# Performance work log

Hardware: AMD Instinct MI355X
Metric: run time of the kernel (lower is better)

## Reference

```python
import jax, jax.numpy as jnp
import numpy as np

EMBED = 1024
D_FF = 4 * EMBED
N_EXPERTS = 8
TOP_K = 2
B, S = 2, 1024


def setup_inputs() -> dict:
    key = jax.random.key(0)
    ks = jax.random.split(key, 10)
    sc_d = 1.0 / np.sqrt(EMBED)
    sc_h = 1.0 / np.sqrt(D_FF)
    return {
        "inputs": jax.random.normal(ks[0], (B, S, EMBED), jnp.float32),
        # router MLP: Linear(D,4D) -> ReLU -> Linear(4D,E)
        "rw1": jax.random.normal(ks[1], (EMBED, D_FF), jnp.float32) * sc_d,
        "rb1": jnp.zeros((D_FF,), jnp.float32),
        "rw2": jax.random.normal(ks[2], (D_FF, N_EXPERTS), jnp.float32) * sc_h,
        "rb2": jnp.zeros((N_EXPERTS,), jnp.float32),
        # stacked expert weights: Linear(D,4D) -> ReLU -> Linear(4D,D)
        "W1": jax.random.normal(ks[3], (N_EXPERTS, EMBED, D_FF), jnp.float32) * sc_d,
        "b1": jnp.zeros((N_EXPERTS, D_FF), jnp.float32),
        "W2": jax.random.normal(ks[4], (N_EXPERTS, D_FF, EMBED), jnp.float32) * sc_h,
        "b2": jnp.zeros((N_EXPERTS, EMBED), jnp.float32),
    }


def reference(inputs, rw1, rb1, rw2, rb2, W1, b1, W2, b2):
    Bb, Ss, D = inputs.shape
    T = Bb * Ss
    xf = inputs.reshape(T, D)  # [T, D]

    # Router: scores over experts, keep top-k, softmax over kept entries only.
    score = jax.nn.relu(xf @ rw1 + rb1) @ rw2 + rb2          # [T, E]
    _, topi = jax.lax.top_k(score, TOP_K)                    # [T, K]
    mask = jnp.zeros(score.shape, bool).at[jnp.arange(T)[:, None], topi].set(True)
    gate = jax.nn.softmax(jnp.where(mask, score, -jnp.inf), axis=-1)  # [T, E]

    # Dense per-expert MLP weighted by gate; gate==0 for non-top-k experts,
    # matching the original masked gather/scatter exactly.
    out = jnp.zeros_like(xf)
    for e in range(N_EXPERTS):
        h = jax.nn.relu(xf @ W1[e] + b1[e])                  # [T, 4D]
        y = h @ W2[e] + b2[e]                                # [T, D]
        out = out + gate[:, e:e + 1] * y
    return out.reshape(Bb, Ss, D)
```

## Files before the change

### kernel.cpp

```cpp
#include <hip/hip_runtime.h>
#include <stdint.h>

typedef unsigned short ushort_t;
typedef __attribute__((ext_vector_type(8))) short short8;
typedef __attribute__((ext_vector_type(4))) float f32x4;

#define EMBED   1024
#define DFF     4096
#define NEXP    8
#define TOKENS  2048
#define SLOTS   4096
#define TMAX    40
#define TG      ((TMAX + 7) / 8)

__device__ __forceinline__ ushort_t f2bf(float f) {
  unsigned u = __float_as_uint(f);
  u += 0x7FFFu + ((u >> 16) & 1u);
  return (ushort_t)(u >> 16);
}
__device__ __forceinline__ float bf2f(ushort_t b) {
  return __uint_as_float(((unsigned)b) << 16);
}

__device__ __forceinline__ void gl2lds16(const void* g, void* l) {
  typedef const __attribute__((address_space(1))) unsigned char* gp_t;
  typedef __attribute__((address_space(3))) unsigned char* lp_t;
  __builtin_amdgcn_global_load_lds((gp_t)(uintptr_t)g, (lp_t)(uintptr_t)l, 16, 0, 0);
}

__device__ __forceinline__ void transp_body(const float* __restrict__ src,
                                            ushort_t* __restrict__ dst,
                                            int src_ld, int dst_ld, int bx, int by,
                                            int dst_koff, int lo, float (*t)[65])
{
  int n0 = bx * 64, k0 = by * 64;
  int tid = threadIdx.x;
  int kk = tid >> 4, nn = (tid & 15) * 4;
  #pragma unroll
  for (int it = 0; it < 4; it++) {
    float4 v = *(const float4*)(src + (size_t)(k0 + kk + it * 16) * src_ld + n0 + nn);
    t[kk + it * 16][nn]     = v.x;
    t[kk + it * 16][nn + 1] = v.y;
    t[kk + it * 16][nn + 2] = v.z;
    t[kk + it * 16][nn + 3] = v.w;
  }
  __syncthreads();
  int nn2 = tid >> 3, kk2 = (tid & 7) * 8;
  #pragma unroll
  for (int it = 0; it < 2; it++) {
    int n = nn2 + it * 32;
    union { ushort_t u[8]; uint4 v; } pk;
    #pragma unroll
    for (int j = 0; j < 8; j++) {
      float xv = t[kk2 + j][n];
      ushort_t hv = f2bf(xv);
      pk.u[j] = lo ? f2bf(xv - bf2f(hv)) : hv;
    }
    *(uint4*)(dst + (size_t)(n0 + n) * dst_ld + dst_koff + k0 + kk2) = pk.v;
  }
}

__global__ void transp_conv(const float* __restrict__ src, ushort_t* __restrict__ dst,
                            int src_ld, int dst_ld, long src_estride, long dst_estride,
                            int dst_koff, int lo)
{
  __shared__ __align__(16) float t[64][65];
  transp_body(src + (size_t)blockIdx.z * src_estride,
              dst + (size_t)blockIdx.z * dst_estride,
              src_ld, dst_ld, blockIdx.x, blockIdx.y, dst_koff, lo, t);
}

__global__ __launch_bounds__(256) void prep_kernel(const float* __restrict__ x,
    ushort_t* __restrict__ Xs, const float* __restrict__ rw1,
    ushort_t* __restrict__ RW1t, int* __restrict__ counts)
{
  __shared__ __align__(16) float tt[64][65];
  int bid = blockIdx.x;
  if (bid < TOKENS) {
    if (bid == 0 && threadIdx.x < NEXP) counts[threadIdx.x] = 0;
    int d = threadIdx.x * 4;
    float4 v = *(const float4*)(x + (size_t)bid * EMBED + d);
    ushort4 hi, lo;
    hi.x = f2bf(v.x); lo.x = f2bf(v.x - bf2f(hi.x));
    hi.y = f2bf(v.y); lo.y = f2bf(v.y - bf2f(hi.y));
    hi.z = f2bf(v.z); lo.z = f2bf(v.z - bf2f(hi.z));
    hi.w = f2bf(v.w); lo.w = f2bf(v.w - bf2f(hi.w));
    ushort_t* row = Xs + (size_t)bid * 2048;
    *(ushort4*)(row + d)        = hi;
    *(ushort4*)(row + 1024 + d) = lo;
    return;
  }
  int idx = bid - TOKENS;
  int n0 = (idx & 63) * 64, k0 = (idx >> 6) * 64;
  int tid = threadIdx.x;
  int kk = tid >> 4, nn = (tid & 15) * 4;
  #pragma unroll
  for (int it = 0; it < 4; it++) {
    float4 v = *(const float4*)(rw1 + (size_t)(k0 + kk + it * 16) * DFF + n0 + nn);
    tt[kk + it * 16][nn]     = v.x;
    tt[kk + it * 16][nn + 1] = v.y;
    tt[kk + it * 16][nn + 2] = v.z;
    tt[kk + it * 16][nn + 3] = v.w;
  }
  __syncthreads();
  int nn2 = tid >> 3, kk2 = (tid & 7) * 8;
  #pragma unroll
  for (int it = 0; it < 2; it++) {
    int n = nn2 + it * 32;
    union { ushort_t u[8]; uint4 v; } ph, pl;
    #pragma unroll
    for (int j = 0; j < 8; j++) {
      float xv = tt[kk2 + j][n];
      ushort_t hv = f2bf(xv);
      ph.u[j] = hv;
      pl.u[j] = f2bf(xv - bf2f(hv));
    }
    ushort_t* row = RW1t + (size_t)(n0 + n) * 3072 + k0 + kk2;
    *(uint4*)(row)        = ph.v;
    *(uint4*)(row + 1024) = ph.v;
    *(uint4*)(row + 2048) = pl.v;
  }
}

template<int APATH, int OUTMODE, bool RELU, bool EXPERT, int SPLITK, int NX, int TSHAPE>
__global__ __launch_bounds__(256, 3)
void gemm_kernel(const ushort_t* __restrict__ A, const ushort_t* __restrict__ B,
                 const float* __restrict__ bias, void* __restrict__ Cout,
                 const float* __restrict__ slot_gate, const int* __restrict__ slot_token,
                 const int* __restrict__ off, const int* __restrict__ tile_e,
                 const int* __restrict__ tile_y, int e0, int e1,
                 int M, int N, int K, int ngb,
                 const float* __restrict__ tsrc, ushort_t* __restrict__ tdst)
{
  __shared__ __align__(16) char lds_raw[49152];
  auto As = (ushort_t(*)[4096])lds_raw;
  auto Bs = (ushort_t(*)[4096])(lds_raw + 24576);

  if constexpr (TSHAPE > 0) {
    int bidf = blockIdx.x;
    if (bidf >= ngb) {
      int idx = bidf - ngb;
      auto tt = (float(*)[65])lds_raw;
      const size_t ES = (size_t)EMBED * DFF;
      if constexpr (TSHAPE == 1) {
        int bx = idx & 63, by = (idx >> 6) & 15, z = idx >> 10;
        transp_body(tsrc + z * ES, tdst + z * ES, DFF, EMBED, bx, by, 0, 0, tt);
      } else {
        int bx = idx & 15, by = (idx >> 4) & 63, z = idx >> 10;
        transp_body(tsrc + z * ES, tdst + z * ES, EMBED, DFF, bx, by, 0, 0, tt);
      }
      return;
    }
  }

  int e = 0, kc = 0, row0, col0, m_base, m_cnt;
  if (EXPERT) {
    constexpr int INNER = NX * SPLITK;
    int bid = blockIdx.x;
    int xcd = bid & 7;
    int j   = bid >> 3;
    int t   = xcd + 8 * (j / INNER);
    int i   = j % INNER;
    int xi  = i % NX;
    kc      = i / NX;
    e = tile_e[t];
    if (e < e0 || e >= e1) return;
    row0   = tile_y[t] * 128;
    col0   = xi * 128;
    m_base = off[e];
    m_cnt  = off[e + 1] - m_base;
  } else {
    int bid = blockIdx.x;
    row0 = (bid >> 5) * 128;
    col0 = (bid & 31) * 128;
    m_base = 0; m_cnt = M;
    if (row0 >= m_cnt) return;
  }
  const int Kc   = K / SPLITK;
  const int kbeg = kc * Kc;

  const int tid  = threadIdx.x;
  const int lane = tid & 63;
  const int wid  = tid >> 6;
  const int wm = wid & 1, wn = wid >> 1;

  const int srow  = lane >> 2;
  const int schk8 = ((lane & 3) ^ ((lane >> 3) & 3)) * 8;

  const ushort_t* gA[2];
  const ushort_t* gB[2];
  int aoff[2];
  const ushort_t* Bt = B + (EXPERT ? (size_t)(e - e0) * (size_t)N * K : 0);
  #pragma unroll
  for (int h = 0; h < 2; h++) {
    int r  = row0 + h * 64 + wid * 16 + srow;
    int rl = min(r, m_cnt - 1);
    size_t rowb;
    if (APATH == 2)      rowb = (size_t)slot_token[m_base + rl] * 2048;
    else if (APATH == 1) rowb = (size_t)rl * 2048;
    else                 rowb = (size_t)(m_base + rl) * (size_t)K;
    gA[h]   = A + rowb + (APATH == 0 ? kbeg : 0) + schk8;
    aoff[h] = (h * 64 + wid * 16) * 32;

    int n = col0 + h * 64 + wid * 16 + srow;
    gB[h] = Bt + (size_t)n * K + kbeg + schk8;
  }

  auto stage = [&](int pb, int kt) {
    const int k0 = kt << 5;
    const int k0a = (APATH == 1 && k0 >= 2048) ? k0 - 2048 : k0;
    #pragma unroll
    for (int h = 0; h < 2; h++) {
      gl2lds16(gA[h] + k0a, &As[pb][aoff[h]]);
      gl2lds16(gB[h] + k0,  &Bs[pb][aoff[h]]);
    }
  };

  f32x4 acc[4][4];
  #pragma unroll
  for (int i = 0; i < 4; i++)
    #pragma unroll
    for (int j = 0; j < 4; j++)
      acc[i][j] = (f32x4){0.f, 0.f, 0.f, 0.f};

  const int q  = lane >> 4;
  const int rr = lane & 15;
  const int sw8 = (q ^ ((rr >> 1) & 3)) * 8;
  const int abase = (wm * 64 + rr) * 32 + sw8;
  const int bbase = (wn * 64 + rr) * 32 + sw8;

  const int nkt = Kc >> 5;

  stage(0, 0);
  if (nkt > 1) stage(1, 1);

  for (int kt = 0; kt < nkt; kt++) {
    if (kt + 1 < nkt) asm volatile("s_waitcnt vmcnt(4)" ::: "memory");
    else              asm volatile("s_waitcnt vmcnt(0)" ::: "memory");
    __builtin_amdgcn_s_barrier();
    __builtin_amdgcn_sched_barrier(0);
    if (kt + 2 < nkt) stage((kt + 2) % 3, kt + 2);

    const int cur = kt % 3;
    short8 af[4], bfr[4];
    #pragma unroll
    for (int i = 0; i < 4; i++) {
      af[i]  = *(const short8*)(&As[cur][abase + i * 512]);
      bfr[i] = *(const short8*)(&Bs[cur][bbase + i * 512]);
    }
    asm volatile("s_waitcnt lgkmcnt(0)" ::: "memory");
    __builtin_amdgcn_sched_barrier(0);
    #pragma unroll
    for (int mt = 0; mt < 4; mt++)
      #pragma unroll
      for (int nt = 0; nt < 4; nt++)
        acc[mt][nt] = __builtin_amdgcn_mfma_f32_16x16x32_bf16(af[mt], bfr[nt], acc[mt][nt], 0, 0, 0);
  }

  const float* biasp = bias + (EXPERT ? (size_t)e * N : 0);
  float bv[4];
  #pragma unroll
  for (int nt = 0; nt < 4; nt++)
    bv[nt] = biasp[col0 + wn * 64 + nt * 16 + rr];
  const float bscale = (SPLITK == 1 || kc == 0) ? 1.f : 0.f;

  if constexpr (OUTMODE == 4) {
    const float* rw2p = slot_gate;
    float4 wa[4], wb[4];
    #pragma unroll
    for (int nt = 0; nt < 4; nt++) {
      int c = col0 + wn * 64 + nt * 16 + rr;
      wa[nt] = *(const float4*)(rw2p + (size_t)c * 8);
      wb[nt] = *(const float4*)(rw2p + (size_t)c * 8 + 4);
    }
    float* Ps = (float*)Cout;
    const int xi2 = (col0 >> 6) + wn;
    #pragma unroll
    for (int mt = 0; mt < 4; mt++) {
      #pragma unroll
      for (int i = 0; i < 4; i++) {
        float4 sA = {0.f, 0.f, 0.f, 0.f}, sB = {0.f, 0.f, 0.f, 0.f};
        #pragma unroll
        for (int nt = 0; nt < 4; nt++) {
          float v = acc[mt][nt][i] + bv[nt];
          if (RELU) v = fmaxf(v, 0.f);
          sA.x += v * wa[nt].x; sA.y += v * wa[nt].y;
          sA.z += v * wa[nt].z; sA.w += v * wa[nt].w;
          sB.x += v * wb[nt].x; sB.y += v * wb[nt].y;
          sB.z += v * wb[nt].z; sB.w += v * wb[nt].w;
        }
        #pragma unroll
        for (int o = 1; o <= 8; o <<= 1) {
          sA.x += __shfl_xor(sA.x, o); sA.y += __shfl_xor(sA.y, o);
          sA.z += __shfl_xor(sA.z, o); sA.w += __shfl_xor(sA.w, o);
          sB.x += __shfl_xor(sB.x, o); sB.y += __shfl_xor(sB.y, o);
          sB.z += __shfl_xor(sB.z, o); sB.w += __shfl_xor(sB.w, o);
        }
        if (rr == 0) {
          int row = row0 + wm * 64 + mt * 16 + q * 4 + i;
          float* p = Ps + ((size_t)row * 64 + xi2) * 8;
          *(float4*)p       = sA;
          *(float4*)(p + 4) = sB;
        }
      }
    }
  } else {
    #pragma unroll
    for (int mt = 0; mt < 4; mt++) {
      #pragma unroll
      for (int i = 0; i < 4; i++) {
        int r_loc = row0 + wm * 64 + mt * 16 + q * 4 + i;
        if (r_loc < m_cnt) {
          int slot = m_base + r_loc;
          float g = 1.f;
          if (OUTMODE == 3) g = slot_gate[slot];
          #pragma unroll
          for (int nt = 0; nt < 4; nt++) {
            float v = acc[mt][nt][i] + bscale * bv[nt];
            if (RELU) v = fmaxf(v, 0.f);
            int c = col0 + wn * 64 + nt * 16 + rr;
            if (OUTMODE == 0)      ((float*)Cout)[(size_t)slot * N + c]    = v;
            else if (OUTMODE == 1) ((ushort_t*)Cout)[(size_t)slot * N + c] = f2bf(v);
            else ((float*)Cout)[((size_t)kc * SLOTS + slot) * N + c] = g * v;
          }
        }
      }
    }
  }
}

__global__ void router_reduce(const float* __restrict__ Ps, const float* __restrict__ rb2,
                              int* __restrict__ topi, float* __restrict__ gates,
                              int* __restrict__ counts)
{
  int t = blockIdx.x * 4 + (threadIdx.x >> 6);
  if (t >= TOKENS) return;
  int lane = threadIdx.x & 63;
  const float* pt = Ps + (size_t)t * 512;
  float4 v0 = *(const float4*)(pt + lane * 8);
  float4 v1 = *(const float4*)(pt + lane * 8 + 4);
  #pragma unroll
  for (int o = 1; o <= 32; o <<= 1) {
    v0.x += __shfl_xor(v0.x, o); v0.y += __shfl_xor(v0.y, o);
    v0.z += __shfl_xor(v0.z, o); v0.w += __shfl_xor(v0.w, o);
    v1.x += __shfl_xor(v1.x, o); v1.y += __shfl_xor(v1.y, o);
    v1.z += __shfl_xor(v1.z, o); v1.w += __shfl_xor(v1.w, o);
  }
  if (lane == 0) {
    float s[8] = {v0.x + rb2[0], v0.y + rb2[1], v0.z + rb2[2], v0.w + rb2[3],
                  v1.x + rb2[4], v1.y + rb2[5], v1.z + rb2[6], v1.w + rb2[7]};
    int i0 = 0;
    #pragma unroll
    for (int e = 1; e < 8; e++) if (s[e] > s[i0]) i0 = e;
    int i1 = (i0 == 0) ? 1 : 0;
    #pragma unroll
    for (int e = 0; e < 8; e++) if (e != i0 && s[e] > s[i1]) i1 = e;
    float ex = __expf(s[i1] - s[i0]);
    float g0 = 1.f / (1.f + ex);
    float g1 = ex / (1.f + ex);
    topi[t * 2] = i0; topi[t * 2 + 1] = i1;
    gates[t * 2] = g0; gates[t * 2 + 1] = g1;
    atomicAdd(&counts[i0], 1);
    atomicAdd(&counts[i1], 1);
  }
}

__global__ void assign_all(const int* __restrict__ counts, const int* __restrict__ topi,
                           const float* __restrict__ gates, int* __restrict__ off,
                           int* __restrict__ tile_e, int* __restrict__ tile_y,
                           int* __restrict__ slot_token, float* __restrict__ slot_gate,
                           int* __restrict__ tok_slot)
{
  __shared__ int s_off[NEXP];
  __shared__ int s_cur[NEXP];
  int tid = threadIdx.x;
  if (tid < NEXP) s_cur[tid] = 0;
  if (tid == 0) {
    int a = 0, t = 0;
    for (int e = 0; e < NEXP; e++) {
      off[e] = a; s_off[e] = a;
      int c = counts[e]; a += c;
      int ty = (c + 127) >> 7;
      for (int y = 0; y < ty; y++) { tile_e[t] = e; tile_y[t] = y; t++; }
    }
    off[NEXP] = a;
    for (; t < TMAX; t++) { tile_e[t] = -1; tile_y[t] = 0; }
  }
  __syncthreads();
  for (int t = tid; t < TOKENS; t += 256) {
    #pragma unroll
    for (int k = 0; k < 2; k++) {
      int e = topi[t * 2 + k];
      int p = atomicAdd(&s_cur[e], 1);
      int s = s_off[e] + p;
      slot_token[s] = t;
      slot_gate[s]  = gates[t * 2 + k];
      tok_slot[t * 2 + k] = s;
    }
  }
}

template<int NC>
__global__ void combine_out(const float* __restrict__ Ys, const int* __restrict__ tok_slot,
                            float* __restrict__ out)
{
  int t = blockIdx.x;
  int d = threadIdx.x * 4;
  int s0 = tok_slot[t * 2], s1 = tok_slot[t * 2 + 1];
  float4 o = {0.f, 0.f, 0.f, 0.f};
  #pragma unroll
  for (int k = 0; k < NC; k++) {
    float4 a = *(const float4*)(Ys + ((size_t)k * SLOTS + s0) * EMBED + d);
    float4 b = *(const float4*)(Ys + ((size_t)k * SLOTS + s1) * EMBED + d);
    o.x += a.x + b.x;
    o.y += a.y + b.y;
    o.z += a.z + b.z;
    o.w += a.w + b.w;
  }
  *(float4*)(out + (size_t)t * EMBED + d) = o;
}

extern "C" void kernel_launch(void* const* d_in, const int* in_sizes, int n_in,
                              void* d_out, int out_size, void* d_ws, size_t ws_size,
                              hipStream_t stream)
{
  const float* x   = (const float*)d_in[0];
  const float* rw1 = (const float*)d_in[1];
  const float* rb1 = (const float*)d_in[2];
  const float* rw2 = (const float*)d_in[3];
  const float* rb2 = (const float*)d_in[4];
  const float* W1  = (const float*)d_in[5];
  const float* b1  = (const float*)d_in[6];
  const float* W2  = (const float*)d_in[7];
  const float* b2  = (const float*)d_in[8];
  float* out = (float*)d_out;
  char* ws = (char*)d_ws;

  const long W1ES = (long)EMBED * DFF;
  const long W2ES = (long)DFF * EMBED;
  const size_t SZ_R = (size_t)4096 * 4096 * 2;

  const bool FULL = ws_size >= ((size_t)300 << 20);

  if (FULL) {
    char* p = ws;
    ushort_t* W1T  = (ushort_t*)p;  p += (size_t)NEXP * DFF * EMBED * 2;
    ushort_t* W2T  = (ushort_t*)p;  p += (size_t)NEXP * EMBED * DFF * 2;
    ushort_t* RW1t = (ushort_t*)p;  p += (size_t)4096 * 3072 * 2;
    ushort_t* Hs   = (ushort_t*)p;  p += (size_t)SLOTS * DFF * 2;
    ushort_t* Xhl  = (ushort_t*)p;  p += (size_t)TOKENS * 2048 * 2;
    float*    Ys   = (float*)p;     p += (size_t)2 * SLOTS * EMBED * 4;
    float*    Ps   = (float*)p;     p += (size_t)TOKENS * 512 * 4;
    int*   topi       = (int*)p;    p += TOKENS * 2 * 4;
    float* gates      = (float*)p;  p += TOKENS * 2 * 4;
    int*   tok_slot   = (int*)p;    p += TOKENS * 2 * 4;
    int*   slot_token = (int*)p;    p += SLOTS * 4;
    float* slot_gate  = (float*)p;  p += SLOTS * 4;
    int*   counts     = (int*)p;    p += 256;
    int*   off        = (int*)p;    p += 256;
    int*   tile_e     = (int*)p;    p += 256;
    int*   tile_y     = (int*)p;    p += 256;

    prep_kernel<<<TOKENS + 1024, 256, 0, stream>>>(x, Xhl, rw1, RW1t, counts);

    gemm_kernel<1, 4, true, false, 1, 32, 1>
        <<<dim3(512 + 8192, 1, 1), 256, 0, stream>>>(Xhl, RW1t, rb1, Ps, rw2,
            nullptr, nullptr, nullptr, nullptr, 0, NEXP, TOKENS, DFF, 3072,
            512, W1, W1T);

    router_reduce<<<512, 256, 0, stream>>>(Ps, rb2, topi, gates, counts);
    assign_all<<<1, 256, 0, stream>>>(counts, topi, gates, off, tile_e, tile_y,
                                      slot_token, slot_gate, tok_slot);

    gemm_kernel<2, 1, true, true, 1, 32, 2>
        <<<dim3(8 * TG * 32 + 8192, 1, 1), 256, 0, stream>>>(Xhl, W1T, b1, Hs,
            nullptr, slot_token, off, tile_e, tile_y, 0, NEXP, 0, DFF, EMBED,
            8 * TG * 32, W2, W2T);

    gemm_kernel<0, 3, false, true, 2, 8, 0>
        <<<dim3(8 * TG * 16, 1, 1), 256, 0, stream>>>(Hs, W2T, b2, Ys,
            slot_gate, nullptr, off, tile_e, tile_y, 0, NEXP, 0, EMBED, DFF,
            0, nullptr, nullptr);

    combine_out<2><<<TOKENS, 256, 0, stream>>>(Ys, tok_slot, out);
  } else {
    ushort_t* RW1t = (ushort_t*)ws;
    ushort_t* WT   = (ushort_t*)ws;
    ushort_t* Hs   = (ushort_t*)(ws + SZ_R);
    ushort_t* Xhl  = (ushort_t*)(ws + 2 * SZ_R);
    float*    Ys   = (float*)(ws + 2 * SZ_R);
    char* p = ws + 3 * SZ_R;
    float* Ps         = (float*)p;  p += (size_t)TOKENS * 512 * 4;
    int*   topi       = (int*)p;    p += TOKENS * 2 * 4;
    float* gates      = (float*)p;  p += TOKENS * 2 * 4;
    int*   tok_slot   = (int*)p;    p += TOKENS * 2 * 4;
    int*   slot_token = (int*)p;    p += SLOTS * 4;
    float* slot_gate  = (float*)p;  p += SLOTS * 4;
    int*   counts     = (int*)p;    p += 256;
    int*   off        = (int*)p;    p += 256;
    int*   tile_e     = (int*)p;    p += 256;
    int*   tile_y     = (int*)p;    p += 256;

    prep_kernel<<<TOKENS + 1024, 256, 0, stream>>>(x, Xhl, rw1, RW1t, counts);

    gemm_kernel<1, 4, true, false, 1, 32, 0>
        <<<dim3(512, 1, 1), 256, 0, stream>>>(Xhl, RW1t, rb1, Ps, rw2, nullptr,
            nullptr, nullptr, nullptr, 0, NEXP, TOKENS, DFF, 3072,
            0, nullptr, nullptr);
    router_reduce<<<512, 256, 0, stream>>>(Ps, rb2, topi, gates, counts);
    assign_all<<<1, 256, 0, stream>>>(counts, topi, gates, off, tile_e, tile_y,
                                      slot_token, slot_gate, tok_slot);

    for (int half = 0; half < 2; half++) {
      int e0 = half * 4;
      transp_conv<<<dim3(64, 16, 4), 256, 0, stream>>>(W1 + (size_t)e0 * W1ES, WT,
          DFF, EMBED, W1ES, W1ES, 0, 0);
      gemm_kernel<2, 1, true, true, 1, 32, 0>
          <<<dim3(8 * TG * 32, 1, 1), 256, 0, stream>>>(Xhl, WT, b1, Hs,
              nullptr, slot_token, off, tile_e, tile_y, e0, e0 + 4, 0, DFF, EMBED,
              0, nullptr, nullptr);
    }
    for (int half = 0; half < 2; half++) {
      int e0 = half * 4;
      transp_conv<<<dim3(16, 64, 4), 256, 0, stream>>>(W2 + (size_t)e0 * W2ES, WT,
          EMBED, DFF, W2ES, W2ES, 0, 0);
      gemm_kernel<0, 3, false, true, 2, 8, 0>
          <<<dim3(8 * TG * 16, 1, 1), 256, 0, stream>>>(Hs, WT, b2, Ys,
              slot_gate, nullptr, off, tile_e, tile_y, e0, e0 + 4, 0, EMBED, DFF,
              0, nullptr, nullptr);
    }

    combine_out<2><<<TOKENS, 256, 0, stream>>>(Ys, tok_slot, out);
  }
}
```

Before: 553.9 us.

## Fuse router top-k and slot assignment into router GEMM via last-block atomics

Removes the separate router_reduce and assign_all launches. The last of each 32-block group of the router GEMM, detected with an atomic counter, reduces partial scores and does top-2 and gating for its 128 tokens. The last of those 16 group-finisher blocks then builds the expert offsets, tile lists and slot maps. This saves two kernel launches and their serialization gaps, at the cost of a serial tail on a few blocks. It also relies on threadfence ordering and counters reset in prep_kernel.

New measurement: 657.3 us. 1.19x slower.

```diff
diff --git a/kernel.cpp b/kernel.cpp
--- a/kernel.cpp
+++ b/kernel.cpp
@@ -77,7 +77,7 @@
   __shared__ __align__(16) float tt[64][65];
   int bid = blockIdx.x;
   if (bid < TOKENS) {
-    if (bid == 0 && threadIdx.x < NEXP) counts[threadIdx.x] = 0;
+    if (bid == 0 && threadIdx.x < 64) counts[threadIdx.x] = 0;
     int d = threadIdx.x * 4;
     float4 v = *(const float4*)(x + (size_t)bid * EMBED + d);
     ushort4 hi, lo;
@@ -130,9 +130,13 @@
                  const int* __restrict__ off, const int* __restrict__ tile_e,
                  const int* __restrict__ tile_y, int e0, int e1,
                  int M, int N, int K, int ngb,
-                 const float* __restrict__ tsrc, ushort_t* __restrict__ tdst)
+                 const float* __restrict__ tsrc, ushort_t* __restrict__ tdst,
+                 const float* __restrict__ r_rb2, int* r_topi, float* r_gates,
+                 int* r_tok_slot, int* r_slot_token, float* r_slot_gate,
+                 int* r_counts, int* r_off, int* r_tile_e, int* r_tile_y)
 {
   __shared__ __align__(16) char lds_raw[49152];
+  __shared__ int s_role;
   auto As = (ushort_t(*)[4096])lds_raw;
   auto Bs = (ushort_t(*)[4096])(lds_raw + 24576);
 
@@ -304,6 +308,78 @@
         }
       }
     }
+
+    __threadfence();
+    __syncthreads();
+    const int rg = (int)(blockIdx.x >> 5);
+    if (tid == 0)
+      s_role = (atomicAdd(&r_counts[16 + rg], 1) == 31);
+    __syncthreads();
+    if (s_role) {
+      __threadfence();
+      for (int it = 0; it < 32; it++) {
+        int t = rg * 128 + it * 4 + (tid >> 6);
+        const float* pt = Ps + (size_t)t * 512;
+        float4 v0 = *(const float4*)(pt + lane * 8);
+        float4 v1 = *(const float4*)(pt + lane * 8 + 4);
+        #pragma unroll
+        for (int o = 1; o <= 32; o <<= 1) {
+          v0.x += __shfl_xor(v0.x, o); v0.y += __shfl_xor(v0.y, o);
+          v0.z += __shfl_xor(v0.z, o); v0.w += __shfl_xor(v0.w, o);
+          v1.x += __shfl_xor(v1.x, o); v1.y += __shfl_xor(v1.y, o);
+          v1.z += __shfl_xor(v1.z, o); v1.w += __shfl_xor(v1.w, o);
+        }
+        if (lane == 0) {
+          float s[8] = {v0.x + r_rb2[0], v0.y + r_rb2[1], v0.z + r_rb2[2], v0.w + r_rb2[3],
+                        v1.x + r_rb2[4], v1.y + r_rb2[5], v1.z + r_rb2[6], v1.w + r_rb2[7]};
+          int i0 = 0;
+          #pragma unroll
+          for (int ee = 1; ee < 8; ee++) if (s[ee] > s[i0]) i0 = ee;
+          int i1 = (i0 == 0) ? 1 : 0;
+          #pragma unroll
+          for (int ee = 0; ee < 8; ee++) if (ee != i0 && s[ee] > s[i1]) i1 = ee;
+          float ex = __expf(s[i1] - s[i0]);
+          r_topi[t * 2] = i0; r_topi[t * 2 + 1] = i1;
+          r_gates[t * 2] = 1.f / (1.f + ex); r_gates[t * 2 + 1] = ex / (1.f + ex);
+          atomicAdd(&r_counts[i0], 1);
+          atomicAdd(&r_counts[i1], 1);
+        }
+      }
+      __threadfence();
+      __syncthreads();
+      if (tid == 0)
+        s_role = (atomicAdd(&r_counts[32], 1) == 15);
+      __syncthreads();
+      if (s_role) {
+        __threadfence();
+        int* s_off = (int*)lds_raw;
+        int* s_cur = (int*)lds_raw + 8;
+        if (tid < NEXP) s_cur[tid] = 0;
+        if (tid == 0) {
+          int a = 0, t = 0;
+          for (int ee = 0; ee < NEXP; ee++) {
+            r_off[ee] = a; s_off[ee] = a;
+            int c = r_counts[ee]; a += c;
+            int ty = (c + 127) >> 7;
+            for (int y = 0; y < ty; y++) { r_tile_e[t] = ee; r_tile_y[t] = y; t++; }
+          }
+          r_off[NEXP] = a;
+          for (; t < TMAX; t++) { r_tile_e[t] = -1; r_tile_y[t] = 0; }
+        }
+        __syncthreads();
+        for (int t = tid; t < TOKENS; t += 256) {
+          #pragma unroll
+          for (int k = 0; k < 2; k++) {
+            int ee = r_topi[t * 2 + k];
+            int pp = atomicAdd(&s_cur[ee], 1);
+            int s = s_off[ee] + pp;
+            r_slot_token[s] = t;
+            r_slot_gate[s]  = r_gates[t * 2 + k];
+            r_tok_slot[t * 2 + k] = s;
+          }
+        }
+      }
+    }
   } else {
     #pragma unroll
     for (int mt = 0; mt < 4; mt++) {
@@ -325,77 +401,6 @@
           }
         }
       }
-    }
-  }
-}
-
-__global__ void router_reduce(const float* __restrict__ Ps, const float* __restrict__ rb2,
-                              int* __restrict__ topi, float* __restrict__ gates,
-                              int* __restrict__ counts)
-{
-  int t = blockIdx.x * 4 + (threadIdx.x >> 6);
-  if (t >= TOKENS) return;
-  int lane = threadIdx.x & 63;
-  const float* pt = Ps + (size_t)t * 512;
-  float4 v0 = *(const float4*)(pt + lane * 8);
-  float4 v1 = *(const float4*)(pt + lane * 8 + 4);
-  #pragma unroll
-  for (int o = 1; o <= 32; o <<= 1) {
-    v0.x += __shfl_xor(v0.x, o); v0.y += __shfl_xor(v0.y, o);
-    v0.z += __shfl_xor(v0.z, o); v0.w += __shfl_xor(v0.w, o);
-    v1.x += __shfl_xor(v1.x, o); v1.y += __shfl_xor(v1.y, o);
-    v1.z += __shfl_xor(v1.z, o); v1.w += __shfl_xor(v1.w, o);
-  }
-  if (lane == 0) {
-    float s[8] = {v0.x + rb2[0], v0.y + rb2[1], v0.z + rb2[2], v0.w + rb2[3],
-                  v1.x + rb2[4], v1.y + rb2[5], v1.z + rb2[6], v1.w + rb2[7]};
-    int i0 = 0;
-    #pragma unroll
-    for (int e = 1; e < 8; e++) if (s[e] > s[i0]) i0 = e;
-    int i1 = (i0 == 0) ? 1 : 0;
-    #pragma unroll
-    for (int e = 0; e < 8; e++) if (e != i0 && s[e] > s[i1]) i1 = e;
-    float ex = __expf(s[i1] - s[i0]);
-    float g0 = 1.f / (1.f + ex);
-    float g1 = ex / (1.f + ex);
-    topi[t * 2] = i0; topi[t * 2 + 1] = i1;
-    gates[t * 2] = g0; gates[t * 2 + 1] = g1;
-    atomicAdd(&counts[i0], 1);
-    atomicAdd(&counts[i1], 1);
-  }
-}
-
-__global__ void assign_all(const int* __restrict__ counts, const int* __restrict__ topi,
-                           const float* __restrict__ gates, int* __restrict__ off,
-                           int* __restrict__ tile_e, int* __restrict__ tile_y,
-                           int* __restrict__ slot_token, float* __restrict__ slot_gate,
-                           int* __restrict__ tok_slot)
-{
-  __shared__ int s_off[NEXP];
-  __shared__ int s_cur[NEXP];
-  int tid = threadIdx.x;
-  if (tid < NEXP) s_cur[tid] = 0;
-  if (tid == 0) {
-    int a = 0, t = 0;
-    for (int e = 0; e < NEXP; e++) {
-      off[e] = a; s_off[e] = a;
-      int c = counts[e]; a += c;
-      int ty = (c + 127) >> 7;
-      for (int y = 0; y < ty; y++) { tile_e[t] = e; tile_y[t] = y; t++; }
-    }
-    off[NEXP] = a;
-    for (; t < TMAX; t++) { tile_e[t] = -1; tile_y[t] = 0; }
-  }
-  __syncthreads();
-  for (int t = tid; t < TOKENS; t += 256) {
-    #pragma unroll
-    for (int k = 0; k < 2; k++) {
-      int e = topi[t * 2 + k];
-      int p = atomicAdd(&s_cur[e], 1);
-      int s = s_off[e] + p;
-      slot_token[s] = t;
-      slot_gate[s]  = gates[t * 2 + k];
-      tok_slot[t * 2 + k] = s;
     }
   }
 }
@@ -466,21 +471,23 @@
     gemm_kernel<1, 4, true, false, 1, 32, 1>
         <<<dim3(512 + 8192, 1, 1), 256, 0, stream>>>(Xhl, RW1t, rb1, Ps, rw2,
             nullptr, nullptr, nullptr, nullptr, 0, NEXP, TOKENS, DFF, 3072,
-            512, W1, W1T);
-
-    router_reduce<<<512, 256, 0, stream>>>(Ps, rb2, topi, gates, counts);
-    assign_all<<<1, 256, 0, stream>>>(counts, topi, gates, off, tile_e, tile_y,
-                                      slot_token, slot_gate, tok_slot);
+            512, W1, W1T,
+            rb2, topi, gates, tok_slot, slot_token, slot_gate, counts,
+            off, tile_e, tile_y);
 
     gemm_kernel<2, 1, true, true, 1, 32, 2>
         <<<dim3(8 * TG * 32 + 8192, 1, 1), 256, 0, stream>>>(Xhl, W1T, b1, Hs,
             nullptr, slot_token, off, tile_e, tile_y, 0, NEXP, 0, DFF, EMBED,
-            8 * TG * 32, W2, W2T);
+            8 * TG * 32, W2, W2T,
+            nullptr, nullptr, nullptr, nullptr, nullptr, nullptr, nullptr,
+            nullptr, nullptr, nullptr);
 
     gemm_kernel<0, 3, false, true, 2, 8, 0>
         <<<dim3(8 * TG * 16, 1, 1), 256, 0, stream>>>(Hs, W2T, b2, Ys,
             slot_gate, nullptr, off, tile_e, tile_y, 0, NEXP, 0, EMBED, DFF,
-            0, nullptr, nullptr);
+            0, nullptr, nullptr,
+            nullptr, nullptr, nullptr, nullptr, nullptr, nullptr, nullptr,
+            nullptr, nullptr, nullptr);
 
     combine_out<2><<<TOKENS, 256, 0, stream>>>(Ys, tok_slot, out);
   } else {
@@ -506,10 +513,9 @@
     gemm_kernel<1, 4, true, false, 1, 32, 0>
         <<<dim3(512, 1, 1), 256, 0, stream>>>(Xhl, RW1t, rb1, Ps, rw2, nullptr,
             nullptr, nullptr, nullptr, 0, NEXP, TOKENS, DFF, 3072,
-            0, nullptr, nullptr);
-    router_reduce<<<512, 256, 0, stream>>>(Ps, rb2, topi, gates, counts);
-    assign_all<<<1, 256, 0, stream>>>(counts, topi, gates, off, tile_e, tile_y,
-                                      slot_token, slot_gate, tok_slot);
+            0, nullptr, nullptr,
+            rb2, topi, gates, tok_slot, slot_token, slot_gate, counts,
+            off, tile_e, tile_y);
 
     for (int half = 0; half < 2; half++) {
       int e0 = half * 4;
@@ -518,7 +524,9 @@
       gemm_kernel<2, 1, true, true, 1, 32, 0>
           <<<dim3(8 * TG * 32, 1, 1), 256, 0, stream>>>(Xhl, WT, b1, Hs,
               nullptr, slot_token, off, tile_e, tile_y, e0, e0 + 4, 0, DFF, EMBED,
-              0, nullptr, nullptr);
+              0, nullptr, nullptr,
+              nullptr, nullptr, nullptr, nullptr, nullptr, nullptr, nullptr,
+              nullptr, nullptr, nullptr);
     }
     for (int half = 0; half < 2; half++) {
       int e0 = half * 4;
@@ -527,7 +535,9 @@
       gemm_kernel<0, 3, false, true, 2, 8, 0>
           <<<dim3(8 * TG * 16, 1, 1), 256, 0, stream>>>(Hs, WT, b2, Ys,
               slot_gate, nullptr, off, tile_e, tile_y, e0, e0 + 4, 0, EMBED, DFF,
-              0, nullptr, nullptr);
+              0, nullptr, nullptr,
+              nullptr, nullptr, nullptr, nullptr, nullptr, nullptr, nullptr,
+              nullptr, nullptr, nullptr);
     }
 
     combine_out<2><<<TOKENS, 256, 0, stream>>>(Ys, tok_slot, out);
```
